# Performance work log

Measured on AMD Instinct MI355X. Metric: run time of the kernel, lower is better.

The kernel has to match this reference:

```python
import jax, jax.numpy as jnp
import numpy as np

DIM = 1536
DEPTH = 8
HEADS = 8
KV_HEADS = 1
GROUPS = HEADS // KV_HEADS
DQK = 128
DV = 192
DIM_PW = 128
POOL = 16
FF_INNER = int(DIM * 2.0)
SOFTCLAMP = 5.0
SCALE = 64 ** -0.5  # source uses default dim_head=64 for scale, not dim_head_qk
MAX_POS = 8192
EPS = float(jnp.finfo(jnp.float32).eps)


def rmsnorm(x, g):
    return x * jax.lax.rsqrt(jnp.mean(x * x, axis=-1, keepdims=True) + EPS) * g


def rotate_half(x):
    x1, x2 = jnp.split(x, 2, axis=-1)
    return jnp.concatenate([-x2, x1], axis=-1)


def apply_rope(pos, t):
    return t * jnp.cos(pos) + rotate_half(t) * jnp.sin(pos)


def rotary_emb(seq_len):
    nf = DQK // 2
    # torch.logspace(1, MAX_POS-nf+1, nf) = 10**linspace -> overflows to inf in fp32 (faithful)
    inv_freq = 1.0 / (jnp.arange(nf, dtype=jnp.float32) + 10.0 ** jnp.linspace(1.0, MAX_POS - nf + 1, nf, dtype=jnp.float32))
    freqs = jnp.arange(seq_len, dtype=jnp.float32)[:, None] * inv_freq[None, :]
    return jnp.concatenate([freqs, freqs], axis=-1)  # [n, DQK]


def softclamp(t, value=SOFTCLAMP):
    return jnp.tanh(t / value) * value


def attention(x, pairwise, rope, w_qkv, qg, kg, vg, bg, w_bias, w_out):
    b, n, _ = x.shape
    qkv = x @ w_qkv
    q, k, v = jnp.split(qkv, [HEADS * DQK, HEADS * DQK + DQK], axis=-1)
    # b n (g h d) -> b g h n d
    q = q.reshape(b, n, GROUPS, KV_HEADS, DQK).transpose(0, 2, 3, 1, 4)
    k = k.reshape(b, n, KV_HEADS, DQK).transpose(0, 2, 1, 3)
    v = v.reshape(b, n, KV_HEADS, DV).transpose(0, 2, 1, 3)
    q = rmsnorm(q, qg)
    k = rmsnorm(k, kg)
    v = rmsnorm(v, vg)
    q = q * SCALE
    q = apply_rope(rope, q)
    k = apply_rope(rope, k)
    sim = jnp.einsum('bghid,bhjd->bghij', q, k)
    # pairwise bias: RMSNorm -> GELU -> Linear(dim_pw, heads) -> b g h i j
    pb = jax.nn.gelu(rmsnorm(pairwise, bg), approximate=False) @ w_bias  # [b, i, j, heads]
    bi = pb.shape[1]
    bias = pb.reshape(b, bi, bi, GROUPS, KV_HEADS).transpose(0, 3, 4, 1, 2)
    bias = jnp.repeat(jnp.repeat(bias, POOL, axis=3), POOL, axis=4)  # expand to seq res
    sim = softclamp(sim + bias)
    attn = jax.nn.softmax(sim, axis=-1)
    out = jnp.einsum('bghij,bhjd->bghid', attn, v)
    out = out.transpose(0, 3, 1, 2, 4).reshape(b, n, GROUPS * KV_HEADS * DV)
    return out @ w_out


def tower(x, pairwise, w_qkv, q_gamma, k_gamma, v_gamma, bias_gamma, w_bias, w_out, attn_pre_gamma, ff_pre_gamma, w_ff1, b_ff1, w_ff2, b_ff2):
    rope = rotary_emb(x.shape[1])
    for d in range(DEPTH):
        xn = rmsnorm(x, attn_pre_gamma[d])
        x = x + attention(xn, pairwise, rope, w_qkv[d], q_gamma[d], k_gamma[d], v_gamma[d], bias_gamma[d], w_bias[d], w_out[d])
        xn = rmsnorm(x, ff_pre_gamma[d])
        x = x + (jax.nn.relu(xn @ w_ff1[d] + b_ff1[d]) @ w_ff2[d] + b_ff2[d])
    return x


def setup_inputs() -> dict:
    key = jax.random.key(0)
    ks = jax.random.split(key, 10)
    s = 0.02
    inp = {
        'x': jax.random.normal(ks[0], (2, 2048, DIM), jnp.float32),
        'pairwise': jax.random.normal(ks[1], (2, 128, 128, DIM_PW), jnp.float32),
        'w_qkv': jax.random.normal(ks[2], (DEPTH, DIM, HEADS * DQK + DQK + DV), jnp.float32) * s,
        'q_gamma': jnp.ones((DEPTH, DQK), jnp.float32),
        'k_gamma': jnp.ones((DEPTH, DQK), jnp.float32),
        'v_gamma': jnp.ones((DEPTH, DV), jnp.float32),
        'bias_gamma': jnp.ones((DEPTH, DIM_PW), jnp.float32),
        'w_bias': jax.random.normal(ks[3], (DEPTH, DIM_PW, HEADS), jnp.float32) * s,
        'w_out': jax.random.normal(ks[4], (DEPTH, DV * HEADS, DIM), jnp.float32) * s,
        'attn_pre_gamma': jnp.ones((DEPTH, DIM), jnp.float32),
        'ff_pre_gamma': jnp.ones((DEPTH, DIM), jnp.float32),
        'w_ff1': jax.random.normal(ks[5], (DEPTH, DIM, FF_INNER), jnp.float32) * s,
        'b_ff1': jnp.zeros((DEPTH, FF_INNER), jnp.float32),
        'w_ff2': jax.random.normal(ks[6], (DEPTH, FF_INNER, DIM), jnp.float32) * s,
        'b_ff2': jnp.zeros((DEPTH, DIM), jnp.float32),
    }
    return inp


def reference(x, pairwise, w_qkv, q_gamma, k_gamma, v_gamma, bias_gamma, w_bias, w_out, attn_pre_gamma, ff_pre_gamma, w_ff1, b_ff1, w_ff2, b_ff2):
    return tower(x, pairwise, w_qkv, q_gamma, k_gamma, v_gamma, bias_gamma, w_bias, w_out, attn_pre_gamma, ff_pre_gamma, w_ff1, b_ff1, w_ff2, b_ff2)
```

## Files before the change

kernel.cpp:

```cpp
#include <hip/hip_runtime.h>

typedef __bf16 bf16;
typedef float f32x4 __attribute__((ext_vector_type(4)));
typedef __bf16 bf16x8 __attribute__((ext_vector_type(8)));
typedef __bf16 bf16x4 __attribute__((ext_vector_type(4)));

#define EPSF 1.1920928955078125e-07f

#define GLOAD_LDS16(gsrc, ldst) \
  __builtin_amdgcn_global_load_lds((const __attribute__((address_space(1))) void*)(gsrc), \
                                   (__attribute__((address_space(3))) void*)(ldst), 16, 0, 0)

__device__ __forceinline__ float wave_reduce_sum(float v) {
#pragma unroll
  for (int m = 1; m < 64; m <<= 1) v += __shfl_xor(v, m, 64);
  return v;
}

__global__ __launch_bounds__(256) void wcast_t(const float* __restrict__ src,
                                               bf16* __restrict__ dst, int R, int C) {
  __shared__ float t[32][33];
  int z = blockIdx.z;
  const float* s = src + (size_t)z * R * C;
  bf16* d = dst + (size_t)z * R * C;
  int c0 = blockIdx.x * 32, r0 = blockIdx.y * 32;
  int tx = threadIdx.x, ty = threadIdx.y;
#pragma unroll
  for (int k = 0; k < 4; ++k)
    t[ty + k * 8][tx] = s[(size_t)(r0 + ty + k * 8) * C + c0 + tx];
  __syncthreads();
#pragma unroll
  for (int k = 0; k < 4; ++k)
    d[(size_t)(c0 + ty + k * 8) * R + r0 + tx] = (bf16)t[tx][ty + k * 8];
}

__global__ __launch_bounds__(256) void rmsnorm_k(const float* __restrict__ X,
                                                 const float* __restrict__ G,
                                                 bf16* __restrict__ O) {
  int row = blockIdx.x, tid = threadIdx.x, lane = tid & 63, w = tid >> 6;
  const float* x = X + (size_t)row * 1536;
  float v[6];
  float ss = 0.f;
#pragma unroll
  for (int k = 0; k < 6; ++k) { v[k] = x[tid + k * 256]; ss += v[k] * v[k]; }
  ss = wave_reduce_sum(ss);
  __shared__ float wsum[4];
  if (lane == 0) wsum[w] = ss;
  __syncthreads();
  ss = wsum[0] + wsum[1] + wsum[2] + wsum[3];
  float rs = rsqrtf(ss * (1.f / 1536.f) + EPSF);
  bf16* o = O + (size_t)row * 1536;
#pragma unroll
  for (int k = 0; k < 6; ++k) o[tid + k * 256] = (bf16)(v[k] * rs * G[tid + k * 256]);
}

template <int EPI>
__global__ __launch_bounds__(256, 3) void gemm_bt(const bf16* __restrict__ A,
                                                  const bf16* __restrict__ Bt,
                                                  float* __restrict__ Cf,
                                                  bf16* __restrict__ Cb,
                                                  const float* __restrict__ bias,
                                                  int M, int N, int K) {
  __shared__ __align__(16) char As[128 * 128];
  __shared__ __align__(16) char Bs[128 * 128];
  const int tid = threadIdx.x;
  const int lane = tid & 63, l15 = lane & 15, l4 = lane >> 4;
  const int w = tid >> 6;
  const int nwg = gridDim.x * gridDim.y;
  const int bid = blockIdx.y * gridDim.x + blockIdx.x;
  const int cpx = nwg >> 3;
  const int swz = (bid & 7) * cpx + (bid >> 3);
  const int rm = (swz / gridDim.x) * 128;
  const int cn = (swz % gridDim.x) * 128;
  const int wm = (w >> 1) * 64, wn = (w & 1) * 64;
  f32x4 acc[4][4] = {};

  for (int kk = 0; kk < K; kk += 64) {
#pragma unroll
    for (int r = 0; r < 4; ++r) {
      uint32_t o = (uint32_t)(r * 256 + tid) * 16;
      uint32_t row = o >> 7;
      uint32_t kb = ((o >> 4) & 7) ^ (row & 7);
      const bf16* src = A + (size_t)(rm + (int)row) * K + kk + kb * 8;
      GLOAD_LDS16(src, As + (o & 0xFFFFFC00u));
    }
#pragma unroll
    for (int r = 0; r < 4; ++r) {
      uint32_t o = (uint32_t)(r * 256 + tid) * 16;
      uint32_t row = o >> 7;
      uint32_t kb = ((o >> 4) & 7) ^ (row & 7);
      int nrow = cn + (int)row;
      if (nrow >= N) nrow = N - 1;
      const bf16* src = Bt + (size_t)nrow * K + kk + kb * 8;
      GLOAD_LDS16(src, Bs + (o & 0xFFFFFC00u));
    }
    __syncthreads();
#pragma unroll
    for (int s = 0; s < 2; ++s) {
      bf16x8 a[4], b[4];
#pragma unroll
      for (int m = 0; m < 4; ++m) {
        uint32_t row = wm + m * 16 + l15;
        uint32_t kb = (uint32_t)(s * 4 + l4);
        a[m] = *(const bf16x8*)(As + row * 128 + (kb ^ (row & 7)) * 16);
      }
#pragma unroll
      for (int n = 0; n < 4; ++n) {
        uint32_t row = wn + n * 16 + l15;
        uint32_t kb = (uint32_t)(s * 4 + l4);
        b[n] = *(const bf16x8*)(Bs + row * 128 + (kb ^ (row & 7)) * 16);
      }
      __builtin_amdgcn_s_setprio(1);
#pragma unroll
      for (int m = 0; m < 4; ++m)
#pragma unroll
        for (int n = 0; n < 4; ++n)
          acc[m][n] = __builtin_amdgcn_mfma_f32_16x16x32_bf16(a[m], b[n], acc[m][n], 0, 0, 0);
      __builtin_amdgcn_s_setprio(0);
    }
    __syncthreads();
  }

#pragma unroll
  for (int m = 0; m < 4; ++m)
#pragma unroll
    for (int n = 0; n < 4; ++n)
#pragma unroll
      for (int r = 0; r < 4; ++r) {
        int row = rm + wm + m * 16 + l4 * 4 + r;
        int col = cn + wn + n * 16 + l15;
        if (col < N) {
          float v = acc[m][n][r];
          size_t idx = (size_t)row * N + col;
          if constexpr (EPI == 2) {
            Cf[idx] += v;
          } else if constexpr (EPI == 3) {
            float tv = v + bias[col];
            Cb[idx] = (bf16)(tv > 0.f ? tv : 0.f);
          } else if constexpr (EPI == 4) {
            Cf[idx] += v + bias[col];
          } else if constexpr (EPI == 5) {
            Cb[idx] = (bf16)v;
          }
        }
      }
}

template <int EPI>
__global__ __launch_bounds__(256, 3) void gemm_bt64(const bf16* __restrict__ A,
                                                    const bf16* __restrict__ Bt,
                                                    float* __restrict__ Cf,
                                                    bf16* __restrict__ Cb,
                                                    const float* __restrict__ bias,
                                                    int M, int N, int K) {
  __shared__ __align__(16) char As[64 * 256];
  __shared__ __align__(16) char Bs[128 * 256];
  const int tid = threadIdx.x;
  const int lane = tid & 63, l15 = lane & 15, l4 = lane >> 4;
  const int w = tid >> 6;
  const int nwg = gridDim.x * gridDim.y;
  const int bid = blockIdx.y * gridDim.x + blockIdx.x;
  const int cpx = nwg >> 3;
  const int swz = (bid & 7) * cpx + (bid >> 3);
  const int rm = (swz / gridDim.x) * 64;
  const int cn = (swz % gridDim.x) * 128;
  const int wm = (w >> 1) * 32, wn = (w & 1) * 64;
  f32x4 acc[2][4] = {};

  for (int kk = 0; kk < K; kk += 128) {
#pragma unroll
    for (int r = 0; r < 4; ++r) {
      uint32_t o = (uint32_t)(r * 256 + tid) * 16;
      uint32_t row = o >> 8;
      uint32_t kb = ((o >> 4) & 15) ^ (row & 15);
      const bf16* src = A + (size_t)(rm + (int)row) * K + kk + kb * 8;
      GLOAD_LDS16(src, As + (o & 0xFFFFF800u) + ((o & 0x7F0u)));
    }
#pragma unroll
    for (int r = 0; r < 8; ++r) {
      uint32_t o = (uint32_t)(r * 256 + tid) * 16;
      uint32_t row = o >> 8;
      uint32_t kb = ((o >> 4) & 15) ^ (row & 15);
      int nrow = cn + (int)row;
      if (nrow >= N) nrow = N - 1;
      const bf16* src = Bt + (size_t)nrow * K + kk + kb * 8;
      GLOAD_LDS16(src, Bs + (o & 0xFFFFF800u) + ((o & 0x7F0u)));
    }
    __syncthreads();
#pragma unroll
    for (int s = 0; s < 4; ++s) {
      bf16x8 a[2], b[4];
#pragma unroll
      for (int m = 0; m < 2; ++m) {
        uint32_t row = wm + m * 16 + l15;
        uint32_t kb = (uint32_t)(s * 4 + l4);
        a[m] = *(const bf16x8*)(As + row * 256 + ((kb ^ (row & 15)) * 16));
      }
#pragma unroll
      for (int n = 0; n < 4; ++n) {
        uint32_t row = wn + n * 16 + l15;
        uint32_t kb = (uint32_t)(s * 4 + l4);
        b[n] = *(const bf16x8*)(Bs + row * 256 + ((kb ^ (row & 15)) * 16));
      }
      __builtin_amdgcn_s_setprio(1);
#pragma unroll
      for (int m = 0; m < 2; ++m)
#pragma unroll
        for (int n = 0; n < 4; ++n)
          acc[m][n] = __builtin_amdgcn_mfma_f32_16x16x32_bf16(a[m], b[n], acc[m][n], 0, 0, 0);
      __builtin_amdgcn_s_setprio(0);
    }
    __syncthreads();
  }

#pragma unroll
  for (int m = 0; m < 2; ++m)
#pragma unroll
    for (int n = 0; n < 4; ++n)
#pragma unroll
      for (int r = 0; r < 4; ++r) {
        int row = rm + wm + m * 16 + l4 * 4 + r;
        int col = cn + wn + n * 16 + l15;
        if (col < N) {
          float v = acc[m][n][r];
          size_t idx = (size_t)row * N + col;
          if constexpr (EPI == 2) {
            Cf[idx] += v;
          } else if constexpr (EPI == 3) {
            float tv = v + bias[col];
            Cb[idx] = (bf16)(tv > 0.f ? tv : 0.f);
          } else if constexpr (EPI == 4) {
            Cf[idx] += v + bias[col];
          } else if constexpr (EPI == 5) {
            Cb[idx] = (bf16)v;
          }
        }
      }
}

__global__ void qkv_post(const bf16* __restrict__ qkv, const float* __restrict__ qg,
                         const float* __restrict__ kg, const float* __restrict__ vg,
                         bf16* __restrict__ Qo, bf16* __restrict__ Ko, bf16* __restrict__ Vo) {
  int t = blockIdx.x, seg = blockIdx.y, lane = threadIdx.x;
  int b = t >> 11, n = t & 2047;
  const bf16* base;
  const float* gamma;
  int len;
  if (seg < 8) { base = qkv + (size_t)t * 1344 + seg * 128; gamma = qg; len = 128; }
  else if (seg == 8) { base = qkv + (size_t)t * 1344 + 1024; gamma = kg; len = 128; }
  else { base = qkv + (size_t)t * 1344 + 1152; gamma = vg; len = 192; }
  float v0 = (float)base[lane], v1 = (float)base[lane + 64];
  float v2 = (len == 192) ? (float)base[lane + 128] : 0.f;
  float ss = wave_reduce_sum(v0 * v0 + v1 * v1 + v2 * v2);
  float rs = rsqrtf(ss / (float)len + EPSF);
  float n0 = v0 * rs * gamma[lane];
  float n1 = v1 * rs * gamma[lane + 64];
  if (seg < 8) {
    n0 *= 0.125f; n1 *= 0.125f;
    if (lane == 0) {
      float th = 0.1f * (float)n;
      float c = cosf(th), s_ = sinf(th);
      float r0 = n0 * c - n1 * s_, r1 = n1 * c + n0 * s_;
      n0 = r0; n1 = r1;
    }
    bf16* q = Qo + ((size_t)((b * 8 + seg) * 2048 + n)) * 128;
    q[lane] = (bf16)n0; q[lane + 64] = (bf16)n1;
  } else if (seg == 8) {
    if (lane == 0) {
      float th = 0.1f * (float)n;
      float c = cosf(th), s_ = sinf(th);
      float r0 = n0 * c - n1 * s_, r1 = n1 * c + n0 * s_;
      n0 = r0; n1 = r1;
    }
    bf16* k = Ko + ((size_t)(b * 2048 + n)) * 128;
    k[lane] = (bf16)n0; k[lane + 64] = (bf16)n1;
  } else {
    float n2 = v2 * rs * vg[lane + 128];
    bf16* vp = Vo + ((size_t)(b * 2048 + n)) * 192;
    vp[lane] = (bf16)n0; vp[lane + 64] = (bf16)n1; vp[lane + 128] = (bf16)n2;
  }
}

__global__ __launch_bounds__(256) void vtrans(const bf16* __restrict__ V, bf16* __restrict__ Vt) {
  __shared__ bf16 t[32][33];
  int b = blockIdx.z;
  int j0 = blockIdx.x * 32, d0 = blockIdx.y * 32;
  int tx = threadIdx.x, ty = threadIdx.y;
#pragma unroll
  for (int k = 0; k < 4; ++k)
    t[ty + k * 8][tx] = V[((size_t)b * 2048 + j0 + ty + k * 8) * 192 + d0 + tx];
  __syncthreads();
#pragma unroll
  for (int k = 0; k < 4; ++k)
    Vt[((size_t)b * 192 + d0 + ty + k * 8) * 2048 + j0 + tx] = t[tx][ty + k * 8];
}

__global__ void bias_pw(const float* __restrict__ P, const float* __restrict__ g,
                        const float* __restrict__ Wb, float* __restrict__ Bout) {
  int j = blockIdx.x, i = blockIdx.y, b = blockIdx.z;
  int lane = threadIdx.x;
  const float* p = P + (((size_t)b * 128 + i) * 128 + j) * 128;
  float a0 = p[lane], a1 = p[lane + 64];
  float ss = wave_reduce_sum(a0 * a0 + a1 * a1);
  float rs = rsqrtf(ss * (1.f / 128.f) + EPSF);
  float x0 = a0 * rs * g[lane], x1 = a1 * rs * g[lane + 64];
  float g0 = 0.5f * x0 * (1.f + erff(x0 * 0.70710678118654752f));
  float g1 = 0.5f * x1 * (1.f + erff(x1 * 0.70710678118654752f));
  __shared__ float gs[128];
  gs[lane] = g0; gs[lane + 64] = g1;
  __syncthreads();
  int h = lane & 7;
  float acc = 0.f;
#pragma unroll
  for (int k = 0; k < 16; ++k) {
    int c = (lane >> 3) + k * 8;
    acc += gs[c] * Wb[c * 8 + h];
  }
  acc += __shfl_xor(acc, 8, 64);
  acc += __shfl_xor(acc, 16, 64);
  acc += __shfl_xor(acc, 32, 64);
  if (lane < 8) Bout[(((size_t)b * 8 + lane) * 128 + i) * 128 + j] = acc;
}

__global__ __launch_bounds__(256, 3) void attn_k(const bf16* __restrict__ Q,
                                                 const bf16* __restrict__ Kg,
                                                 const bf16* __restrict__ Vt,
                                                 const float* __restrict__ Bias,
                                                 bf16* __restrict__ Out) {
  __shared__ __align__(16) char Ks[64 * 256];
  __shared__ __align__(16) char Vs[192 * 128];
  __shared__ __align__(16) char Ps[64 * 128];
  __shared__ float BiasS[4 * 128];
  int tid = threadIdx.x, lane = tid & 63, w = tid >> 6;
  int it = blockIdx.x, g = blockIdx.y, b = blockIdx.z;
  int i0 = it * 64;
  int l15 = lane & 15, l4 = lane >> 4;

  bf16x8 qf[4];
#pragma unroll
  for (int s = 0; s < 4; ++s)
    qf[s] = *(const bf16x8*)(Q + ((size_t)((b * 8 + g) * 2048 + i0 + w * 16 + l15)) * 128 + s * 32 + l4 * 8);

  if (tid < 128) {
    int r = tid >> 5, c = (tid & 31) * 4;
    float4 bv = *(const float4*)(Bias + ((size_t)((b * 8 + g) * 128) + (i0 >> 4) + r) * 128 + c);
    bv.x *= 0.57707801635558535f; bv.y *= 0.57707801635558535f;
    bv.z *= 0.57707801635558535f; bv.w *= 0.57707801635558535f;
    *(float4*)&BiasS[r * 128 + c] = bv;
  }

  f32x4 accO[12] = {};
  float lacc = 0.f;

  for (int jt = 0; jt < 32; ++jt) {
    int j0 = jt * 64;
#pragma unroll
    for (int r = 0; r < 4; ++r) {
      uint32_t o = (uint32_t)(r * 256 + tid) * 16;
      uint32_t row = o >> 8;
      uint32_t kb = ((o >> 4) & 15) ^ (row & 15);
      const bf16* src = Kg + ((size_t)b * 2048 + j0 + (int)row) * 128 + kb * 8;
      GLOAD_LDS16(src, Ks + (o & 0xFFFFFC00u));
    }
#pragma unroll
    for (int r = 0; r < 6; ++r) {
      uint32_t o = (uint32_t)(r * 256 + tid) * 16;
      uint32_t dv = o >> 7;
      uint32_t kb = ((o >> 4) & 7) ^ (dv & 7);
      const bf16* src = Vt + ((size_t)b * 192 + dv) * 2048 + j0 + kb * 8;
      GLOAD_LDS16(src, Vs + (o & 0xFFFFFC00u));
    }
    __syncthreads();

    f32x4 accS[4] = {};
#pragma unroll
    for (int s = 0; s < 4; ++s) {
      bf16x8 kf[4];
#pragma unroll
      for (int n = 0; n < 4; ++n) {
        uint32_t row = n * 16 + l15;
        uint32_t kb = (uint32_t)(s * 4 + l4);
        kf[n] = *(const bf16x8*)(Ks + row * 256 + (kb ^ (row & 15)) * 16);
      }
      __builtin_amdgcn_s_setprio(1);
#pragma unroll
      for (int n = 0; n < 4; ++n)
        accS[n] = __builtin_amdgcn_mfma_f32_16x16x32_bf16(kf[n], qf[s], accS[n], 0, 0, 0);
      __builtin_amdgcn_s_setprio(0);
    }

#pragma unroll
    for (int n = 0; n < 4; ++n) {
      float biaS = BiasS[w * 128 + jt * 4 + n];
      bf16x4 pk;
#pragma unroll
      for (int r = 0; r < 4; ++r) {
        float t1 = __builtin_fmaf(0.57707801635558535f, accS[n][r], biaS);
        float e1 = exp2f(t1);
        float rr = __builtin_amdgcn_rcpf(e1 + 1.0f);
        float pv = exp2f(-14.426950408889634f * rr);
        lacc += pv;
        pk[r] = (bf16)pv;
      }
      uint32_t prow = (uint32_t)(w * 16 + l15);
      uint32_t byteo = prow * 128 + (uint32_t)(n * 16 + l4 * 4) * 2;
      byteo ^= (prow & 7) << 4;
      *(bf16x4*)(Ps + byteo) = pk;
    }

#pragma unroll
    for (int s = 0; s < 2; ++s) {
      uint32_t prow = (uint32_t)(w * 16 + l15);
      uint32_t byteo = prow * 128 + (uint32_t)(s * 64 + l4 * 16);
      byteo ^= (prow & 7) << 4;
      bf16x8 pa = *(const bf16x8*)(Ps + byteo);
#pragma unroll
      for (int n = 0; n < 12; ++n) {
        uint32_t dvr = n * 16 + l15;
        uint32_t kb = (uint32_t)(s * 4 + l4);
        bf16x8 vf = *(const bf16x8*)(Vs + dvr * 128 + (kb ^ (dvr & 7)) * 16);
        __builtin_amdgcn_s_setprio(1);
        accO[n] = __builtin_amdgcn_mfma_f32_16x16x32_bf16(vf, pa, accO[n], 0, 0, 0);
        __builtin_amdgcn_s_setprio(0);
      }
    }
    __syncthreads();
  }

  lacc += __shfl_xor(lacc, 16, 64);
  lacc += __shfl_xor(lacc, 32, 64);
  float rl = __builtin_amdgcn_rcpf(lacc);

  {
    int i = i0 + w * 16 + l15;
#pragma unroll
    for (int n = 0; n < 12; ++n) {
      bf16x4 ok;
#pragma unroll
      for (int r = 0; r < 4; ++r) ok[r] = (bf16)(accO[n][r] * rl);
      int dv = n * 16 + l4 * 4;
      *(bf16x4*)(Out + ((size_t)(b * 2048 + i)) * 1536 + g * 192 + dv) = ok;
    }
  }
}

extern "C" void kernel_launch(void* const* d_in, const int* in_sizes, int n_in,
                              void* d_out, int out_size, void* d_ws, size_t ws_size,
                              hipStream_t stream) {
  (void)in_sizes; (void)n_in; (void)out_size;
  const float* x_in = (const float*)d_in[0];
  const float* pairwise = (const float*)d_in[1];
  const float* w_qkv = (const float*)d_in[2];
  const float* q_gamma = (const float*)d_in[3];
  const float* k_gamma = (const float*)d_in[4];
  const float* v_gamma = (const float*)d_in[5];
  const float* bias_gamma = (const float*)d_in[6];
  const float* w_bias = (const float*)d_in[7];
  const float* w_out = (const float*)d_in[8];
  const float* attn_pre = (const float*)d_in[9];
  const float* ff_pre = (const float*)d_in[10];
  const float* w_ff1 = (const float*)d_in[11];
  const float* b_ff1 = (const float*)d_in[12];
  const float* w_ff2 = (const float*)d_in[13];
  const float* b_ff2 = (const float*)d_in[14];

  char* p = (char*)d_ws;
  auto alloc = [&](size_t bytes) {
    char* r = p;
    p += (bytes + 255) & ~(size_t)255;
    return r;
  };
  bf16* wT_qkv = (bf16*)alloc(8ull * 1344 * 1536 * 2);
  bf16* wT_out = (bf16*)alloc(8ull * 1536 * 1536 * 2);
  bf16* wT_ff1 = (bf16*)alloc(8ull * 3072 * 1536 * 2);
  bf16* wT_ff2 = (bf16*)alloc(8ull * 1536 * 3072 * 2);
  float* x_ws = (float*)alloc(4096ull * 1536 * 4);
  bf16* xn = (bf16*)alloc(4096ull * 1536 * 2);
  bf16* qkvb = (bf16*)alloc(4096ull * 1344 * 2);
  bf16* qb = (bf16*)alloc(2ull * 8 * 2048 * 128 * 2);
  bf16* kb = (bf16*)alloc(2ull * 2048 * 128 * 2);
  bf16* vb = (bf16*)alloc(2ull * 2048 * 192 * 2);
  bf16* vtb = (bf16*)alloc(2ull * 192 * 2048 * 2);
  float* biasb = (float*)alloc(2ull * 8 * 128 * 128 * 4);
  bf16* attn_o = (bf16*)alloc(4096ull * 1536 * 2);
  bf16* hb = (bf16*)alloc(4096ull * 3072 * 2);
  if ((size_t)(p - (char*)d_ws) > ws_size) return;

  wcast_t<<<dim3(42, 48, 8), dim3(32, 8), 0, stream>>>(w_qkv, wT_qkv, 1536, 1344);
  wcast_t<<<dim3(48, 48, 8), dim3(32, 8), 0, stream>>>(w_out, wT_out, 1536, 1536);
  wcast_t<<<dim3(96, 48, 8), dim3(32, 8), 0, stream>>>(w_ff1, wT_ff1, 1536, 3072);
  wcast_t<<<dim3(48, 96, 8), dim3(32, 8), 0, stream>>>(w_ff2, wT_ff2, 3072, 1536);

  hipMemcpyAsync(x_ws, x_in, 4096ull * 1536 * 4, hipMemcpyDeviceToDevice, stream);

  for (int d = 0; d < 8; ++d) {
    const bf16* wq = wT_qkv + (size_t)d * 1344 * 1536;
    const bf16* wo = wT_out + (size_t)d * 1536 * 1536;
    const bf16* w1 = wT_ff1 + (size_t)d * 3072 * 1536;
    const bf16* w2 = wT_ff2 + (size_t)d * 1536 * 3072;

    rmsnorm_k<<<4096, 256, 0, stream>>>(x_ws, attn_pre + d * 1536, xn);
    gemm_bt64<5><<<dim3(11, 64), 256, 0, stream>>>(xn, wq, nullptr, qkvb, nullptr, 4096, 1344, 1536);
    qkv_post<<<dim3(4096, 10), 64, 0, stream>>>(qkvb, q_gamma + d * 128, k_gamma + d * 128,
                                                v_gamma + d * 192, qb, kb, vb);
    vtrans<<<dim3(64, 6, 2), dim3(32, 8), 0, stream>>>(vb, vtb);
    bias_pw<<<dim3(128, 128, 2), 64, 0, stream>>>(pairwise, bias_gamma + d * 128,
                                                  w_bias + d * 128 * 8, biasb);
    attn_k<<<dim3(32, 8, 2), 256, 0, stream>>>(qb, kb, vtb, biasb, attn_o);
    gemm_bt64<2><<<dim3(12, 64), 256, 0, stream>>>(attn_o, wo, x_ws, nullptr, nullptr, 4096, 1536, 1536);
    rmsnorm_k<<<4096, 256, 0, stream>>>(x_ws, ff_pre + d * 1536, xn);
    gemm_bt<3><<<dim3(24, 32), 256, 0, stream>>>(xn, w1, nullptr, hb, b_ff1 + d * 3072, 4096, 3072, 1536);
    gemm_bt64<4><<<dim3(12, 64), 256, 0, stream>>>(hb, w2, x_ws, nullptr, b_ff2 + d * 1536, 4096, 1536, 3072);
  }

  hipMemcpyAsync(d_out, x_ws, 4096ull * 1536 * 4, hipMemcpyDeviceToDevice, stream);
}
```

Measured before the change: 2.417 ms.

## Double-buffer gemm_bt64 K loop, hoist pairwise bias for all layers, batch qkv_post

```diff
diff --git a/kernel.cpp b/kernel.cpp
--- a/kernel.cpp
+++ b/kernel.cpp
@@ -153,8 +153,8 @@
                                                     bf16* __restrict__ Cb,
                                                     const float* __restrict__ bias,
                                                     int M, int N, int K) {
-  __shared__ __align__(16) char As[64 * 256];
-  __shared__ __align__(16) char Bs[128 * 256];
+  __shared__ __align__(16) char As[2][64 * 128];
+  __shared__ __align__(16) char Bs[2][128 * 128];
   const int tid = threadIdx.x;
   const int lane = tid & 63, l15 = lane & 15, l4 = lane >> 4;
   const int w = tid >> 6;
@@ -167,40 +167,42 @@
   const int wm = (w >> 1) * 32, wn = (w & 1) * 64;
   f32x4 acc[2][4] = {};
 
-  for (int kk = 0; kk < K; kk += 128) {
+  auto STAGE = [&](int buf, int kk) {
+#pragma unroll
+    for (int r = 0; r < 2; ++r) {
+      uint32_t o = (uint32_t)(r * 256 + tid) * 16;
+      uint32_t row = o >> 7;
+      uint32_t kb = ((o >> 4) & 7) ^ (row & 7);
+      const bf16* src = A + (size_t)(rm + (int)row) * K + kk + kb * 8;
+      GLOAD_LDS16(src, &As[buf][0] + (o & 0xFFFFFC00u));
+    }
 #pragma unroll
     for (int r = 0; r < 4; ++r) {
       uint32_t o = (uint32_t)(r * 256 + tid) * 16;
-      uint32_t row = o >> 8;
-      uint32_t kb = ((o >> 4) & 15) ^ (row & 15);
-      const bf16* src = A + (size_t)(rm + (int)row) * K + kk + kb * 8;
-      GLOAD_LDS16(src, As + (o & 0xFFFFF800u) + ((o & 0x7F0u)));
-    }
-#pragma unroll
-    for (int r = 0; r < 8; ++r) {
-      uint32_t o = (uint32_t)(r * 256 + tid) * 16;
-      uint32_t row = o >> 8;
-      uint32_t kb = ((o >> 4) & 15) ^ (row & 15);
+      uint32_t row = o >> 7;
+      uint32_t kb = ((o >> 4) & 7) ^ (row & 7);
       int nrow = cn + (int)row;
       if (nrow >= N) nrow = N - 1;
       const bf16* src = Bt + (size_t)nrow * K + kk + kb * 8;
-      GLOAD_LDS16(src, Bs + (o & 0xFFFFF800u) + ((o & 0x7F0u)));
-    }
-    __syncthreads();
-#pragma unroll
-    for (int s = 0; s < 4; ++s) {
+      GLOAD_LDS16(src, &Bs[buf][0] + (o & 0xFFFFFC00u));
+    }
+  };
+
+  auto COMPUTE = [&](int buf) {
+#pragma unroll
+    for (int s = 0; s < 2; ++s) {
       bf16x8 a[2], b[4];
 #pragma unroll
       for (int m = 0; m < 2; ++m) {
         uint32_t row = wm + m * 16 + l15;
         uint32_t kb = (uint32_t)(s * 4 + l4);
-        a[m] = *(const bf16x8*)(As + row * 256 + ((kb ^ (row & 15)) * 16));
+        a[m] = *(const bf16x8*)(&As[buf][0] + row * 128 + (kb ^ (row & 7)) * 16);
       }
 #pragma unroll
       for (int n = 0; n < 4; ++n) {
         uint32_t row = wn + n * 16 + l15;
         uint32_t kb = (uint32_t)(s * 4 + l4);
-        b[n] = *(const bf16x8*)(Bs + row * 256 + ((kb ^ (row & 15)) * 16));
+        b[n] = *(const bf16x8*)(&Bs[buf][0] + row * 128 + (kb ^ (row & 7)) * 16);
       }
       __builtin_amdgcn_s_setprio(1);
 #pragma unroll
@@ -210,8 +212,18 @@
           acc[m][n] = __builtin_amdgcn_mfma_f32_16x16x32_bf16(a[m], b[n], acc[m][n], 0, 0, 0);
       __builtin_amdgcn_s_setprio(0);
     }
-    __syncthreads();
-  }
+  };
+
+  STAGE(0, 0);
+  __syncthreads();
+  int cur = 0;
+  for (int kk = 64; kk < K; kk += 64) {
+    STAGE(cur ^ 1, kk);
+    COMPUTE(cur);
+    __syncthreads();
+    cur ^= 1;
+  }
+  COMPUTE(cur);
 
 #pragma unroll
   for (int m = 0; m < 2; ++m)
@@ -238,10 +250,14 @@
       }
 }
 
-__global__ void qkv_post(const bf16* __restrict__ qkv, const float* __restrict__ qg,
-                         const float* __restrict__ kg, const float* __restrict__ vg,
-                         bf16* __restrict__ Qo, bf16* __restrict__ Ko, bf16* __restrict__ Vo) {
-  int t = blockIdx.x, seg = blockIdx.y, lane = threadIdx.x;
+__global__ __launch_bounds__(256) void qkv_post(const bf16* __restrict__ qkv,
+                                                const float* __restrict__ qg,
+                                                const float* __restrict__ kg,
+                                                const float* __restrict__ vg,
+                                                bf16* __restrict__ Qo, bf16* __restrict__ Ko,
+                                                bf16* __restrict__ Vo) {
+  int lane = threadIdx.x & 63, wv = threadIdx.x >> 6;
+  int t = blockIdx.x * 4 + wv, seg = blockIdx.y;
   int b = t >> 11, n = t & 2047;
   const bf16* base;
   const float* gamma;
@@ -295,31 +311,36 @@
     Vt[((size_t)b * 192 + d0 + ty + k * 8) * 2048 + j0 + tx] = t[tx][ty + k * 8];
 }
 
-__global__ void bias_pw(const float* __restrict__ P, const float* __restrict__ g,
-                        const float* __restrict__ Wb, float* __restrict__ Bout) {
+__global__ void bias_pw8(const float* __restrict__ P, const float* __restrict__ G8,
+                         const float* __restrict__ Wb8, float* __restrict__ Bout) {
   int j = blockIdx.x, i = blockIdx.y, b = blockIdx.z;
   int lane = threadIdx.x;
   const float* p = P + (((size_t)b * 128 + i) * 128 + j) * 128;
   float a0 = p[lane], a1 = p[lane + 64];
   float ss = wave_reduce_sum(a0 * a0 + a1 * a1);
   float rs = rsqrtf(ss * (1.f / 128.f) + EPSF);
-  float x0 = a0 * rs * g[lane], x1 = a1 * rs * g[lane + 64];
-  float g0 = 0.5f * x0 * (1.f + erff(x0 * 0.70710678118654752f));
-  float g1 = 0.5f * x1 * (1.f + erff(x1 * 0.70710678118654752f));
+  float pn0 = a0 * rs, pn1 = a1 * rs;
   __shared__ float gs[128];
-  gs[lane] = g0; gs[lane + 64] = g1;
-  __syncthreads();
-  int h = lane & 7;
-  float acc = 0.f;
-#pragma unroll
-  for (int k = 0; k < 16; ++k) {
-    int c = (lane >> 3) + k * 8;
-    acc += gs[c] * Wb[c * 8 + h];
-  }
-  acc += __shfl_xor(acc, 8, 64);
-  acc += __shfl_xor(acc, 16, 64);
-  acc += __shfl_xor(acc, 32, 64);
-  if (lane < 8) Bout[(((size_t)b * 8 + lane) * 128 + i) * 128 + j] = acc;
+  for (int d = 0; d < 8; ++d) {
+    float x0 = pn0 * G8[d * 128 + lane], x1 = pn1 * G8[d * 128 + lane + 64];
+    float g0 = 0.5f * x0 * (1.f + erff(x0 * 0.70710678118654752f));
+    float g1 = 0.5f * x1 * (1.f + erff(x1 * 0.70710678118654752f));
+    __syncthreads();
+    gs[lane] = g0; gs[lane + 64] = g1;
+    __syncthreads();
+    int h = lane & 7;
+    float acc = 0.f;
+#pragma unroll
+    for (int k = 0; k < 16; ++k) {
+      int c = (lane >> 3) + k * 8;
+      acc += gs[c] * Wb8[((size_t)d * 128 + c) * 8 + h];
+    }
+    acc += __shfl_xor(acc, 8, 64);
+    acc += __shfl_xor(acc, 16, 64);
+    acc += __shfl_xor(acc, 32, 64);
+    if (lane < 8)
+      Bout[((((size_t)d * 2 + b) * 8 + lane) * 128 + i) * 128 + j] = acc;
+  }
 }
 
 __global__ __launch_bounds__(256, 3) void attn_k(const bf16* __restrict__ Q,
@@ -481,7 +502,7 @@
   bf16* kb = (bf16*)alloc(2ull * 2048 * 128 * 2);
   bf16* vb = (bf16*)alloc(2ull * 2048 * 192 * 2);
   bf16* vtb = (bf16*)alloc(2ull * 192 * 2048 * 2);
-  float* biasb = (float*)alloc(2ull * 8 * 128 * 128 * 4);
+  float* biasb8 = (float*)alloc(8ull * 2 * 8 * 128 * 128 * 4);
   bf16* attn_o = (bf16*)alloc(4096ull * 1536 * 2);
   bf16* hb = (bf16*)alloc(4096ull * 3072 * 2);
   if ((size_t)(p - (char*)d_ws) > ws_size) return;
@@ -490,6 +511,8 @@
   wcast_t<<<dim3(48, 48, 8), dim3(32, 8), 0, stream>>>(w_out, wT_out, 1536, 1536);
   wcast_t<<<dim3(96, 48, 8), dim3(32, 8), 0, stream>>>(w_ff1, wT_ff1, 1536, 3072);
   wcast_t<<<dim3(48, 96, 8), dim3(32, 8), 0, stream>>>(w_ff2, wT_ff2, 3072, 1536);
+
+  bias_pw8<<<dim3(128, 128, 2), 64, 0, stream>>>(pairwise, bias_gamma, w_bias, biasb8);
 
   hipMemcpyAsync(x_ws, x_in, 4096ull * 1536 * 4, hipMemcpyDeviceToDevice, stream);
 
@@ -501,12 +524,11 @@
 
     rmsnorm_k<<<4096, 256, 0, stream>>>(x_ws, attn_pre + d * 1536, xn);
     gemm_bt64<5><<<dim3(11, 64), 256, 0, stream>>>(xn, wq, nullptr, qkvb, nullptr, 4096, 1344, 1536);
-    qkv_post<<<dim3(4096, 10), 64, 0, stream>>>(qkvb, q_gamma + d * 128, k_gamma + d * 128,
-                                                v_gamma + d * 192, qb, kb, vb);
+    qkv_post<<<dim3(1024, 10), 256, 0, stream>>>(qkvb, q_gamma + d * 128, k_gamma + d * 128,
+                                                 v_gamma + d * 192, qb, kb, vb);
     vtrans<<<dim3(64, 6, 2), dim3(32, 8), 0, stream>>>(vb, vtb);
-    bias_pw<<<dim3(128, 128, 2), 64, 0, stream>>>(pairwise, bias_gamma + d * 128,
-                                                  w_bias + d * 128 * 8, biasb);
-    attn_k<<<dim3(32, 8, 2), 256, 0, stream>>>(qb, kb, vtb, biasb, attn_o);
+    attn_k<<<dim3(32, 8, 2), 256, 0, stream>>>(qb, kb, vtb,
+                                               biasb8 + (size_t)d * 2 * 8 * 128 * 128, attn_o);
     gemm_bt64<2><<<dim3(12, 64), 256, 0, stream>>>(attn_o, wo, x_ws, nullptr, nullptr, 4096, 1536, 1536);
     rmsnorm_k<<<4096, 256, 0, stream>>>(x_ws, ff_pre + d * 1536, xn);
     gemm_bt<3><<<dim3(24, 32), 256, 0, stream>>>(xn, w1, nullptr, hb, b_ff1 + d * 3072, 4096, 3072, 1536);
```

Result: no change. 2.456 ms (+1.6%).
